# Performance work log

Measured on AMD Instinct MI355X. Metric: run time of the kernel, lower is better.

Reference implementation:

```python
import jax, jax.numpy as jnp
import numpy as np

B, T, D = 2, 2048, 1024
NH = 16
HD = D // NH


def setup_inputs() -> dict:
    key = jax.random.key(0)
    ks = jax.random.split(key, 5)
    s = 0.02
    return {
        "x": jax.random.normal(ks[0], (B, T, D), dtype=jnp.float32),
        "Wq": jax.random.normal(ks[1], (D, D), dtype=jnp.float32) * s,
        "Wk": jax.random.normal(ks[2], (D, D), dtype=jnp.float32) * s,
        "Wv": jax.random.normal(ks[3], (D, D), dtype=jnp.float32) * s,
        "Wo": jax.random.normal(ks[4], (D, D), dtype=jnp.float32) * s,
        "bo": jnp.zeros((D,), dtype=jnp.float32),
    }


def reference(x, Wq, Wk, Wv, Wo, bo):
    b, t, _ = x.shape
    scale = HD ** -0.5
    # torch Linear: y = x @ W^T
    q = (x @ Wq.T).reshape(b, t, NH, HD)
    k = (x @ Wk.T).reshape(b, t, NH, HD)
    v = (x @ Wv.T).reshape(b, t, NH, HD)
    # scores: [b, nh, t, t]
    s = jnp.einsum("bqhd,bkhd->bhqk", q, k) * scale
    causal = jnp.tril(jnp.ones((t, t), dtype=bool))
    s = jnp.where(causal, s, -jnp.inf)
    p = jax.nn.softmax(s, axis=-1)
    o = jnp.einsum("bhqk,bkhd->bqhd", p, v).reshape(b, t, D)
    return o @ Wo.T + bo
```

## Files before the change

kernel.cpp:

```cpp
#include <hip/hip_runtime.h>


typedef __bf16 bf16x8 __attribute__((ext_vector_type(8)));
typedef float f32x4 __attribute__((ext_vector_type(4)));
typedef unsigned short ushortx8 __attribute__((ext_vector_type(8)));
typedef unsigned short ushortx4 __attribute__((ext_vector_type(4)));

#define T_SEQ 2048
#define NHEAD 16
#define HDIM 64
#define DMODEL 1024

__device__ inline unsigned short f2bf(float f) {
  unsigned int u = __builtin_bit_cast(unsigned int, f);
  unsigned int r = (u + 0x7fffu + ((u >> 16) & 1u)) >> 16;
  return (unsigned short)r;
}

__device__ inline void gl16(const unsigned short* g, unsigned short* l) {
  __builtin_amdgcn_global_load_lds(
      (const __attribute__((address_space(1))) unsigned int*)g,
      (__attribute__((address_space(3))) unsigned int*)l, 16, 0, 0);
}

__global__ void cast_all(const float* __restrict__ x, const float* __restrict__ w0,
                         const float* __restrict__ w1, const float* __restrict__ w2,
                         const float* __restrict__ w3, unsigned short* __restrict__ out) {
  const int NX = 2 * T_SEQ * DMODEL;
  int i = (blockIdx.x * 256 + threadIdx.x) * 4;
  const float* src;
  int off;
  if (i < NX) {
    src = x; off = i;
  } else {
    const int j = i - NX;
    const int sel = j >> 20;
    off = j & ((1 << 20) - 1);
    src = sel == 0 ? w0 : sel == 1 ? w1 : sel == 2 ? w2 : w3;
  }
  float4 v = *reinterpret_cast<const float4*>(src + off);
  ushortx4 o;
  o[0] = f2bf(v.x); o[1] = f2bf(v.y); o[2] = f2bf(v.z); o[3] = f2bf(v.w);
  *reinterpret_cast<ushortx4*>(out + i) = o;
}

__device__ __forceinline__ void gemm_core(
    const unsigned short* __restrict__ A, const unsigned short* __restrict__ Bw,
    int K, int m0, int n0, f32x4 acc[4][4]) {
  __shared__ unsigned short As[4096];
  __shared__ unsigned short Bs[4096];
  const int tid = threadIdx.x;
  const int lane = tid & 63, wid = tid >> 6;
  const int wr = wid >> 1, wc = wid & 1;
  const int lr = lane & 15, lg = lane >> 4;
  const int srow = tid >> 2;
  const int scs = ((tid & 3) ^ (srow & 3)) * 8;
  const unsigned short* ga0 = A + (size_t)(m0 + srow) * K + scs;
  const unsigned short* gb0 = Bw + (size_t)(n0 + srow) * K + scs;
  unsigned short* la0 = As + tid * 8;
  unsigned short* lb0 = Bs + tid * 8;
  const int rca = (lg ^ (lr & 3)) * 8;

  for (int k0 = 0; k0 < K; k0 += 32) {
    __syncthreads();
    gl16(ga0 + k0, la0);
    gl16(ga0 + (size_t)64 * K + k0, la0 + 2048);
    gl16(gb0 + k0, lb0);
    gl16(gb0 + (size_t)64 * K + k0, lb0 + 2048);
    __syncthreads();

    bf16x8 af[4], bfr[4];
#pragma unroll
    for (int t = 0; t < 4; ++t) {
      af[t]  = *reinterpret_cast<const bf16x8*>(&As[(wr * 64 + t * 16 + lr) * 32 + rca]);
      bfr[t] = *reinterpret_cast<const bf16x8*>(&Bs[(wc * 64 + t * 16 + lr) * 32 + rca]);
    }
#pragma unroll
    for (int mi = 0; mi < 4; ++mi)
#pragma unroll
      for (int ni = 0; ni < 4; ++ni)
        acc[mi][ni] = __builtin_amdgcn_mfma_f32_16x16x32_bf16(af[mi], bfr[ni], acc[mi][ni], 0, 0, 0);
  }
}

__global__ __launch_bounds__(256) void gemm_qkv(
    const unsigned short* __restrict__ xb, const unsigned short* __restrict__ Wall,
    unsigned short* __restrict__ Qb, unsigned short* __restrict__ Kb,
    unsigned short* __restrict__ Vtb) {
  const int z = blockIdx.y;
  const int bid = blockIdx.x;
  int m0, n0;
  const unsigned short* A;
  const unsigned short* Bw;
  if (z < 2) {
    n0 = (bid & 7) * 128; m0 = (bid >> 3) * 128;
    A = xb; Bw = Wall + (size_t)z * (DMODEL * DMODEL);
  } else {
    m0 = (bid & 7) * 128; n0 = (bid >> 3) * 128;
    A = Wall + (size_t)2 * (DMODEL * DMODEL); Bw = xb;
  }
  f32x4 acc[4][4] = {};
  gemm_core(A, Bw, DMODEL, m0, n0, acc);

  const int tid = threadIdx.x, lane = tid & 63, wid = tid >> 6;
  const int wr = wid >> 1, wc = wid & 1, lr = lane & 15, lg = lane >> 4;
  const int mb = m0 + wr * 64, nb = n0 + wc * 64;
  const float scale = z == 0 ? 0.125f * 1.44269504089f : 1.0f;
#pragma unroll
  for (int mi = 0; mi < 4; ++mi)
#pragma unroll
    for (int ni = 0; ni < 4; ++ni) {
      const int col = nb + ni * 16 + lr;
#pragma unroll
      for (int j = 0; j < 4; ++j) {
        const int row = mb + mi * 16 + lg * 4 + j;
        const float v = acc[mi][ni][j] * scale;
        if (z < 2) {
          const int b = row >> 11, t = row & (T_SEQ - 1);
          const int h = col >> 6, d = col & (HDIM - 1);
          unsigned short* out = z == 0 ? Qb : Kb;
          out[(((size_t)(b * NHEAD + h) * T_SEQ + t) << 6) + d] = f2bf(v);
        } else {
          const int h = row >> 6, d = row & (HDIM - 1);
          const int b = col >> 11, t = col & (T_SEQ - 1);
          Vtb[(((size_t)(b * NHEAD + h) * HDIM + d) << 11) + t] = f2bf(v);
        }
      }
    }
}

__global__ __launch_bounds__(256) void gemm_proj(
    const unsigned short* __restrict__ Ob, const unsigned short* __restrict__ Wob,
    float* __restrict__ out, const float* __restrict__ bias) {
  const int m0 = blockIdx.y * 128, n0 = blockIdx.x * 128;
  f32x4 acc[4][4] = {};
  gemm_core(Ob, Wob, DMODEL, m0, n0, acc);

  const int tid = threadIdx.x, lane = tid & 63, wid = tid >> 6;
  const int wr = wid >> 1, wc = wid & 1, lr = lane & 15, lg = lane >> 4;
  const int mb = m0 + wr * 64, nb = n0 + wc * 64;
#pragma unroll
  for (int mi = 0; mi < 4; ++mi)
#pragma unroll
    for (int ni = 0; ni < 4; ++ni) {
      const int col = nb + ni * 16 + lr;
      const float bv = bias[col];
#pragma unroll
      for (int j = 0; j < 4; ++j) {
        const int row = mb + mi * 16 + lg * 4 + j;
        out[(size_t)row * DMODEL + col] = acc[mi][ni][j] + bv;
      }
    }
}

__device__ __forceinline__ void attn_step(
    const unsigned short* Kslot, const unsigned short* Vslot,
    const int kh0, const int kh1, const int (&vo)[2][2],
    const bf16x8 (&qf)[2], f32x4 (&acc)[4], float& mrun, float& lrun,
    const bool domask, const int kb, const int q, const int lg) {
  f32x4 s[4] = {};
  __builtin_amdgcn_s_setprio(1);
#pragma unroll
  for (int c = 0; c < 4; ++c) {
    bf16x8 k0 = *reinterpret_cast<const bf16x8*>(&Kslot[kh0 + c * 1024]);
    bf16x8 k1 = *reinterpret_cast<const bf16x8*>(&Kslot[kh1 + c * 1024]);
    s[c] = __builtin_amdgcn_mfma_f32_16x16x32_bf16(k0, qf[0], s[c], 0, 0, 0);
    s[c] = __builtin_amdgcn_mfma_f32_16x16x32_bf16(k1, qf[1], s[c], 0, 0, 0);
  }
  __builtin_amdgcn_s_setprio(0);
  if (domask) {
#pragma unroll
    for (int c = 0; c < 4; ++c)
#pragma unroll
      for (int j = 0; j < 4; ++j) {
        const int k = kb + c * 16 + lg * 4 + j;
        if (k > q) s[c][j] = -INFINITY;
      }
  }
  float tm = -INFINITY;
#pragma unroll
  for (int c = 0; c < 4; ++c)
#pragma unroll
    for (int j = 0; j < 4; ++j) tm = fmaxf(tm, s[c][j]);
  tm = fmaxf(tm, __shfl_xor(tm, 16, 64));
  tm = fmaxf(tm, __shfl_xor(tm, 32, 64));
  if (!__all(tm <= mrun + 8.f)) {
    const float mnew = fmaxf(mrun, tm);
    const float fac = exp2f(mrun - mnew);
    lrun *= fac;
#pragma unroll
    for (int dt = 0; dt < 4; ++dt)
#pragma unroll
      for (int j = 0; j < 4; ++j) acc[dt][j] *= fac;
    mrun = mnew;
  }
  float tsum = 0.f;
#pragma unroll
  for (int c = 0; c < 4; ++c)
#pragma unroll
    for (int j = 0; j < 4; ++j) {
      const float p = exp2f(s[c][j] - mrun);
      s[c][j] = p;
      tsum += p;
    }
  tsum += __shfl_xor(tsum, 16, 64);
  tsum += __shfl_xor(tsum, 32, 64);
  lrun += tsum;

  bf16x8 pb[2];
#pragma unroll
  for (int ks = 0; ks < 2; ++ks) {
    bf16x8 t8;
#pragma unroll
    for (int e = 0; e < 8; ++e) t8[e] = (__bf16)s[ks * 2 + (e >> 2)][e & 3];
    pb[ks] = t8;
  }
  __builtin_amdgcn_s_setprio(1);
#pragma unroll
  for (int dt = 0; dt < 4; ++dt) {
#pragma unroll
    for (int ks = 0; ks < 2; ++ks) {
      uint2 vlo = *reinterpret_cast<const uint2*>(&Vslot[vo[ks][0] + dt * 1024]);
      uint2 vhi = *reinterpret_cast<const uint2*>(&Vslot[vo[ks][1] + dt * 1024]);
      uint4 u;
      u.x = vlo.x; u.y = vlo.y; u.z = vhi.x; u.w = vhi.y;
      bf16x8 vf = __builtin_bit_cast(bf16x8, u);
      acc[dt] = __builtin_amdgcn_mfma_f32_16x16x32_bf16(vf, pb[ks], acc[dt], 0, 0, 0);
    }
  }
  __builtin_amdgcn_s_setprio(0);
}

__global__ __launch_bounds__(512, 4) void flash_attn(
    const unsigned short* __restrict__ Q, const unsigned short* __restrict__ Kg,
    const unsigned short* __restrict__ Vt, unsigned short* __restrict__ O) {
  __shared__ unsigned short Ks[4][4096];
  __shared__ unsigned short Vs[4][4096];
  const int tid = threadIdx.x, lane = tid & 63, wid = tid >> 6;
  const int lr = lane & 15, lg = lane >> 4, wq = wid & 3;
  const int bid = blockIdx.x;
  const int bh = (bid & 7) * 4 + ((bid >> 3) & 3);
  const int a = (bid >> 5) & 15;
  const int b = 31 - a;
  const bool g0 = wid < 4;
  const int myq1 = g0 ? a : b;
  const int q1 = myq1 * 64 + wq * 16 + lr;
  const int q2 = b * 64 + wq * 16 + lr;
  const size_t base = (size_t)bh * (T_SEQ * HDIM);

  bf16x8 qf1[2], qf2[2];
#pragma unroll
  for (int h = 0; h < 2; ++h) {
    qf1[h] = *reinterpret_cast<const bf16x8*>(Q + base + (size_t)q1 * HDIM + h * 32 + lg * 8);
    qf2[h] = *reinterpret_cast<const bf16x8*>(Q + base + (size_t)q2 * HDIM + h * 32 + lg * 8);
  }

  const int srow = tid >> 3;
  const int schk = ((tid & 7) ^ (srow & 7)) * 8;
  const unsigned short* kst = Kg + base + (size_t)srow * HDIM + schk;
  const unsigned short* vst = Vt + base + (size_t)srow * T_SEQ + schk;

#define STAGE(slot, kt_)                                \
  do {                                                  \
    const int kb_ = (kt_) * 64;                         \
    gl16(kst + (size_t)kb_ * HDIM, &Ks[slot][tid * 8]); \
    gl16(vst + kb_, &Vs[slot][tid * 8]);                \
  } while (0)

  const int kh0 = lr * 64 + (((0 * 4 + lg) ^ (lr & 7)) * 8);
  const int kh1 = lr * 64 + (((1 * 4 + lg) ^ (lr & 7)) * 8);
  int vo[2][2];
#pragma unroll
  for (int ks = 0; ks < 2; ++ks) {
    vo[ks][0] = lr * 64 + (((ks * 4 + (lg >> 1)) ^ (lr & 7)) * 8) + (lg & 1) * 4;
    vo[ks][1] = lr * 64 + (((ks * 4 + 2 + (lg >> 1)) ^ (lr & 7)) * 8) + (lg & 1) * 4;
  }

  float m1 = -INFINITY, l1 = 0.f, m2 = -INFINITY, l2 = 0.f;
  f32x4 acc1[4] = {}, acc2[4] = {};

  STAGE(0, 0);
  asm volatile("s_waitcnt vmcnt(0)" ::: "memory");
  __builtin_amdgcn_s_barrier();
  asm volatile("" ::: "memory");

  for (int kt = 0; kt <= a; ++kt) {
    if (kt < a) {
      STAGE((kt + 1) & 3, kt + 1);
    } else {
      STAGE((a + 1) & 3, a + 1);
      if (a + 2 <= b) STAGE((a + 2) & 3, a + 2);
    }
    attn_step(Ks[kt & 3], Vs[kt & 3], kh0, kh1, vo, qf1, acc1, m1, l1,
              g0 && (kt == a), kt * 64, q1, lg);
    asm volatile("s_waitcnt vmcnt(0)" ::: "memory");
    __builtin_amdgcn_s_barrier();
    asm volatile("" ::: "memory");
  }

  for (int t0 = a + 1; t0 <= b; t0 += 2) {
    if (t0 + 2 <= b) STAGE((t0 + 2) & 3, t0 + 2);
    if (t0 + 3 <= b) STAGE((t0 + 3) & 3, t0 + 3);
    if (!g0) {
      attn_step(Ks[t0 & 3], Vs[t0 & 3], kh0, kh1, vo, qf2, acc1, m1, l1,
                t0 == b, t0 * 64, q2, lg);
    } else if (t0 + 1 <= b) {
      attn_step(Ks[(t0 + 1) & 3], Vs[(t0 + 1) & 3], kh0, kh1, vo, qf2, acc2, m2, l2,
                false, (t0 + 1) * 64, q2, lg);
    }
    asm volatile("s_waitcnt vmcnt(0)" ::: "memory");
    __builtin_amdgcn_s_barrier();
    asm volatile("" ::: "memory");
  }
#undef STAGE

  float* sm = reinterpret_cast<float*>(&Ks[0][0]);
  const int lid = (wq * 64 + lane) * 18;
  if (g0) {
    float* p = sm + lid;
    p[0] = m2; p[1] = l2;
#pragma unroll
    for (int dt = 0; dt < 4; ++dt)
#pragma unroll
      for (int j = 0; j < 4; ++j) p[2 + dt * 4 + j] = acc2[dt][j];
  }
  __syncthreads();
  if (!g0) {
    const float* p = sm + lid;
    const float mo = p[0], lo = p[1];
    const float ms = fmaxf(m1, mo);
    const float f1 = exp2f(m1 - ms), f2 = exp2f(mo - ms);
    l1 = l1 * f1 + lo * f2;
#pragma unroll
    for (int dt = 0; dt < 4; ++dt)
#pragma unroll
      for (int j = 0; j < 4; ++j)
        acc1[dt][j] = acc1[dt][j] * f1 + p[2 + dt * 4 + j] * f2;
  }

  const int b_ = bh >> 4, h_ = bh & (NHEAD - 1);
  const float inv = 1.0f / l1;
  unsigned short* orow = O + (((size_t)(b_ * T_SEQ + q1)) << 10) + h_ * HDIM + lg * 4;
#pragma unroll
  for (int dt = 0; dt < 4; ++dt) {
    ushortx4 o4;
#pragma unroll
    for (int j = 0; j < 4; ++j) o4[j] = f2bf(acc1[dt][j] * inv);
    *reinterpret_cast<ushortx4*>(orow + dt * 16) = o4;
  }
}

extern "C" void kernel_launch(void* const* d_in, const int* in_sizes, int n_in,
                              void* d_out, int out_size, void* d_ws, size_t ws_size,
                              hipStream_t stream) {
  const float* x  = (const float*)d_in[0];
  const float* Wq = (const float*)d_in[1];
  const float* Wk = (const float*)d_in[2];
  const float* Wv = (const float*)d_in[3];
  const float* Wo = (const float*)d_in[4];
  const float* bo = (const float*)d_in[5];
  float* out = (float*)d_out;

  const int M = 2 * T_SEQ;
  const int NXD = DMODEL * DMODEL;
  const int NX = M * DMODEL;

  unsigned short* ws = (unsigned short*)d_ws;
  unsigned short* xb  = ws;
  unsigned short* Wqb = xb + NX;
  unsigned short* Wob = Wqb + 3 * (size_t)NXD;
  unsigned short* Qb  = Wqb + 4 * (size_t)NXD;
  unsigned short* Kbf = Qb + NX;
  unsigned short* Vtb = Kbf + NX;
  unsigned short* Ob  = Vtb + NX;

  cast_all<<<(NX + 4 * NXD) / 1024, 256, 0, stream>>>(x, Wq, Wk, Wv, Wo, xb);

  dim3 gq(256, 3);
  gemm_qkv<<<gq, 256, 0, stream>>>(xb, Wqb, Qb, Kbf, Vtb);

  flash_attn<<<512, 512, 0, stream>>>(Qb, Kbf, Vtb, Ob);

  dim3 gg(DMODEL / 128, M / 128);
  gemm_proj<<<gg, 256, 0, stream>>>(Ob, Wob, out, bo);
}
```

Measured before the change: 113.0 us.

## Deepen K/V prefetch to a 5-slot ring buffer with partial vmcnt waits

Grows the shared-memory K/V staging from 4 to 5 slots and prefetches tiles one step further ahead in both phases of the attention loop. Waits now use vmcnt(2) instead of vmcnt(0), so the newest tile's loads can stay in flight across the barrier and global-load latency is hidden behind MFMA work. In exchange, LDS use per block grows by a quarter, which may cut occupancy under launch_bounds(512,4), and the modular slot indexing adds scalar work and risks ordering bugs.

```diff
diff --git a/kernel.cpp b/kernel.cpp
--- a/kernel.cpp
+++ b/kernel.cpp
@@ -234,8 +234,8 @@
 __global__ __launch_bounds__(512, 4) void flash_attn(
     const unsigned short* __restrict__ Q, const unsigned short* __restrict__ Kg,
     const unsigned short* __restrict__ Vt, unsigned short* __restrict__ O) {
-  __shared__ unsigned short Ks[4][4096];
-  __shared__ unsigned short Vs[4][4096];
+  __shared__ unsigned short Ks[5][4096];
+  __shared__ unsigned short Vs[5][4096];
   const int tid = threadIdx.x, lane = tid & 63, wid = tid >> 6;
   const int lr = lane & 15, lg = lane >> 4, wq = wid & 3;
   const int bid = blockIdx.x;
@@ -280,37 +280,53 @@
   f32x4 acc1[4] = {}, acc2[4] = {};
 
   STAGE(0, 0);
-  asm volatile("s_waitcnt vmcnt(0)" ::: "memory");
+  STAGE(1, 1);
+  asm volatile("s_waitcnt vmcnt(2)" ::: "memory");
   __builtin_amdgcn_s_barrier();
   asm volatile("" ::: "memory");
 
+  int sl = 0;
   for (int kt = 0; kt <= a; ++kt) {
-    if (kt < a) {
-      STAGE((kt + 1) & 3, kt + 1);
+    const int st = kt + 2;
+    int sst = sl + 2; if (sst >= 5) sst -= 5;
+    if (st <= b) STAGE(sst, st);
+    attn_step(Ks[sl], Vs[sl], kh0, kh1, vo, qf1, acc1, m1, l1,
+              g0 && (kt == a), kt * 64, q1, lg);
+    if (kt < a && st <= b) {
+      asm volatile("s_waitcnt vmcnt(2)" ::: "memory");
     } else {
-      STAGE((a + 1) & 3, a + 1);
-      if (a + 2 <= b) STAGE((a + 2) & 3, a + 2);
-    }
-    attn_step(Ks[kt & 3], Vs[kt & 3], kh0, kh1, vo, qf1, acc1, m1, l1,
-              g0 && (kt == a), kt * 64, q1, lg);
-    asm volatile("s_waitcnt vmcnt(0)" ::: "memory");
+      asm volatile("s_waitcnt vmcnt(0)" ::: "memory");
+    }
     __builtin_amdgcn_s_barrier();
     asm volatile("" ::: "memory");
-  }
-
+    ++sl; if (sl >= 5) sl -= 5;
+  }
+
+  {
+    int s3 = sl + 2; if (s3 >= 5) s3 -= 5;
+    if (a + 3 <= b) STAGE(s3, a + 3);
+  }
   for (int t0 = a + 1; t0 <= b; t0 += 2) {
-    if (t0 + 2 <= b) STAGE((t0 + 2) & 3, t0 + 2);
-    if (t0 + 3 <= b) STAGE((t0 + 3) & 3, t0 + 3);
+    int s1 = sl + 1; if (s1 >= 5) s1 -= 5;
+    int s3 = sl + 3; if (s3 >= 5) s3 -= 5;
+    int s4 = sl + 4; if (s4 >= 5) s4 -= 5;
+    if (t0 + 3 <= b) STAGE(s3, t0 + 3);
+    if (t0 + 4 <= b) STAGE(s4, t0 + 4);
     if (!g0) {
-      attn_step(Ks[t0 & 3], Vs[t0 & 3], kh0, kh1, vo, qf2, acc1, m1, l1,
+      attn_step(Ks[sl], Vs[sl], kh0, kh1, vo, qf2, acc1, m1, l1,
                 t0 == b, t0 * 64, q2, lg);
     } else if (t0 + 1 <= b) {
-      attn_step(Ks[(t0 + 1) & 3], Vs[(t0 + 1) & 3], kh0, kh1, vo, qf2, acc2, m2, l2,
+      attn_step(Ks[s1], Vs[s1], kh0, kh1, vo, qf2, acc2, m2, l2,
                 false, (t0 + 1) * 64, q2, lg);
     }
-    asm volatile("s_waitcnt vmcnt(0)" ::: "memory");
+    if (t0 + 4 <= b) {
+      asm volatile("s_waitcnt vmcnt(2)" ::: "memory");
+    } else {
+      asm volatile("s_waitcnt vmcnt(0)" ::: "memory");
+    }
     __builtin_amdgcn_s_barrier();
     asm volatile("" ::: "memory");
+    sl += 2; if (sl >= 5) sl -= 5;
   }
 #undef STAGE
 
```

New measurement: 113.2 us. Within noise of the previous version (+0.2%).
